# Kernel optimization log

Hardware: AMD Instinct MI355X
Metric: run time of the kernel (lower is better)

The kernel has to match this reference:

```python
import jax, jax.numpy as jnp
import numpy as np


def setup_inputs() -> dict:
    key = jax.random.key(0)
    k1, k2, k3, k4 = jax.random.split(key, 4)
    N, E, DIN, H1, H2 = 100000, 1600000, 128, 64, 32
    x = jax.random.normal(k1, (N, DIN), dtype=jnp.float32)
    edge_index = jax.random.randint(k2, (2, E), 0, N, dtype=jnp.int64)
    # Glorot-style scaled init for the two GCN weight matrices (no bias)
    W1 = jax.random.normal(k3, (DIN, H1), dtype=jnp.float32) * (1.0 / np.sqrt(DIN))
    W2 = jax.random.normal(k4, (H1, H2), dtype=jnp.float32) * (1.0 / np.sqrt(H1))
    return {"x": x, "edge_index": edge_index, "W1": W1, "W2": W2}


def reference(x, edge_index, W1, W2):
    N = x.shape[0]
    loop = jnp.arange(N, dtype=edge_index.dtype)
    src = jnp.concatenate([edge_index[0], loop])  # [E+N]
    dst = jnp.concatenate([edge_index[1], loop])  # [E+N]
    # symmetric GCN normalization with self-loops (edge_weight = 1)
    deg = jax.ops.segment_sum(jnp.ones(src.shape, x.dtype), dst, num_segments=N)
    dinv = jnp.where(deg > 0, jax.lax.rsqrt(deg), 0.0)
    norm = dinv[src] * dinv[dst]  # [E+N]

    def gcn_conv(h, W):
        h = h @ W  # transform first (PyG GCNConv order)
        msg = h[src] * norm[:, None]  # gather + scale
        return jax.ops.segment_sum(msg, dst, num_segments=N)  # scatter-add

    hidden1 = jax.nn.relu(gcn_conv(x, W1))
    z = gcn_conv(hidden1, W2)
    return z
```

## Files before the change

kernel.cpp:

```cpp
#include <hip/hip_runtime.h>
#include <hip/hip_fp16.h>

#define DIN 128
#define H1  64
#define H2  32
#define NCH 512
#define BSH 8

typedef _Float16 f16x8 __attribute__((ext_vector_type(8)));
typedef _Float16 f16x4 __attribute__((ext_vector_type(4)));
typedef float    f32x4 __attribute__((ext_vector_type(4)));

__global__ __launch_bounds__(256) void k_hist(const int* __restrict__ dst,
        int* __restrict__ H, int E, int NB, int chunk) {
    __shared__ int lh[512];
    int c = blockIdx.x, tid = threadIdx.x;
    for (int b = tid; b < NB; b += 256) lh[b] = 0;
    __syncthreads();
    int e0 = c * chunk, e1 = min(E, e0 + chunk);
    for (int e = e0 + tid; e < e1; e += 256)
        atomicAdd(&lh[dst[e] >> BSH], 1);
    __syncthreads();
    for (int b = tid; b < NB; b += 256) H[(size_t)b * NCH + c] = lh[b];
}

__global__ __launch_bounds__(256) void k_scan1(const int* __restrict__ in,
        int* __restrict__ out, int* __restrict__ partial, int N) {
    int tid = threadIdx.x;
    int base = blockIdx.x * 1024 + tid * 4;
    int v0 = (base + 0 < N) ? in[base + 0] : 0;
    int v1 = (base + 1 < N) ? in[base + 1] : 0;
    int v2 = (base + 2 < N) ? in[base + 2] : 0;
    int v3 = (base + 3 < N) ? in[base + 3] : 0;
    int sum = v0 + v1 + v2 + v3;
    int lane = tid & 63, wid = tid >> 6;
    int x = sum;
#pragma unroll
    for (int off = 1; off < 64; off <<= 1) {
        int y = __shfl_up(x, off, 64);
        if (lane >= off) x += y;
    }
    __shared__ int wsum[4];
    if (lane == 63) wsum[wid] = x;
    __syncthreads();
    int wbase = 0;
    for (int w = 0; w < wid; ++w) wbase += wsum[w];
    int excl = wbase + x - sum;
    if (base + 0 < N) out[base + 0] = excl;
    if (base + 1 < N) out[base + 1] = excl + v0;
    if (base + 2 < N) out[base + 2] = excl + v0 + v1;
    if (base + 3 < N) out[base + 3] = excl + v0 + v1 + v2;
    if (tid == 0) partial[blockIdx.x] = wsum[0] + wsum[1] + wsum[2] + wsum[3];
}

__global__ __launch_bounds__(256) void k_scan2(int* __restrict__ partial, int nb) {
    int tid = threadIdx.x;
    int v = (tid < nb) ? partial[tid] : 0;
    __shared__ int tmp[256];
    tmp[tid] = v;
    __syncthreads();
    for (int off = 1; off < 256; off <<= 1) {
        int y = (tid >= off) ? tmp[tid - off] : 0;
        __syncthreads();
        tmp[tid] += y;
        __syncthreads();
    }
    if (tid < nb) partial[tid] = tmp[tid] - v;
}

__global__ void k_scan3b(int* __restrict__ a, const int* __restrict__ partial, int n) {
    int i = blockIdx.x * blockDim.x + threadIdx.x;
    if (i < n) a[i] += partial[i >> 10];
}

__global__ __launch_bounds__(256) void k_bsort(const int* __restrict__ src,
        const int* __restrict__ dst, const int* __restrict__ H,
        int* __restrict__ ep, int E, int NB, int chunk) {
    __shared__ int cur[512];
    int c = blockIdx.x, tid = threadIdx.x;
    for (int b = tid; b < NB; b += 256) cur[b] = H[(size_t)b * NCH + c];
    __syncthreads();
    int e0 = c * chunk, e1 = min(E, e0 + chunk);
    for (int e = e0 + tid; e < e1; e += 256) {
        int s = src[e], d = dst[e];
        int pos = atomicAdd(&cur[d >> BSH], 1);
        ep[pos] = s | ((d & ((1 << BSH) - 1)) << 20);
    }
}

__global__ __launch_bounds__(256) void k_csr(const int* __restrict__ ep,
        const int* __restrict__ H, int* __restrict__ degi, int* __restrict__ rowptr,
        float* __restrict__ dinv, int* __restrict__ csr_src, int E, int N, int NB) {
    __shared__ int cnt[256], pos[256], wsum[4];
    int b = blockIdx.x, tid = threadIdx.x;
    int base = b << BSH;
    cnt[tid] = 0;
    int bstart = H[(size_t)b * NCH];
    int bend = (b + 1 < NB) ? H[(size_t)(b + 1) * NCH] : E;
    __syncthreads();
    for (int e = bstart + tid; e < bend; e += 256)
        atomicAdd(&cnt[ep[e] >> 20], 1);
    __syncthreads();
    int v = cnt[tid];
    int lane = tid & 63, wid = tid >> 6;
    int x = v;
#pragma unroll
    for (int off = 1; off < 64; off <<= 1) {
        int y = __shfl_up(x, off, 64);
        if (lane >= off) x += y;
    }
    if (lane == 63) wsum[wid] = x;
    __syncthreads();
    int wbase = 0;
    for (int w = 0; w < wid; ++w) wbase += wsum[w];
    int excl = wbase + x - v;
    int n = base + tid;
    if (n < N) {
        degi[n]   = v;
        dinv[n]   = rsqrtf((float)v + 1.0f);
        rowptr[n] = bstart + excl;
    }
    pos[tid] = bstart + excl;
    __syncthreads();
    for (int e = bstart + tid; e < bend; e += 256) {
        int p = ep[e];
        int q = atomicAdd(&pos[p >> 20], 1);
        csr_src[q] = p & 0xFFFFF;
    }
}

__global__ __launch_bounds__(256) void k_mgemm1(const float* __restrict__ x,
        const float* __restrict__ W1, const float* __restrict__ dinv,
        _Float16* __restrict__ t1h, int N) {
    __shared__ _Float16 sA[64 * 128];
    __shared__ _Float16 sB[64 * 128];
    int tid = threadIdx.x;
    int row0 = blockIdx.x * 64;
#pragma unroll
    for (int i = 0; i < 8; ++i) {
        int idx4 = tid + 256 * i;
        int r = idx4 >> 5, c4 = idx4 & 31;
        int row = row0 + r;
        float4 v = make_float4(0.f, 0.f, 0.f, 0.f);
        if (row < N) v = *(const float4*)&x[(size_t)row * DIN + c4 * 4];
        f16x4 h;
        h[0] = (_Float16)v.x; h[1] = (_Float16)v.y;
        h[2] = (_Float16)v.z; h[3] = (_Float16)v.w;
        int byte = (c4 * 8) ^ ((r & 7) << 4);
        *(f16x4*)((char*)sA + r * 256 + byte) = h;
    }
    {
        int n = tid & 63, kq = tid >> 6;
        _Float16 tmp[32];
#pragma unroll
        for (int kk = 0; kk < 32; ++kk)
            tmp[kk] = (_Float16)W1[(size_t)(kq * 32 + kk) * H1 + n];
#pragma unroll
        for (int j = 0; j < 4; ++j) {
            int byte = ((kq * 32 + j * 8) * 2) ^ ((n & 7) << 4);
            *(f16x8*)((char*)sB + n * 256 + byte) = *(f16x8*)&tmp[j * 8];
        }
    }
    __syncthreads();
    int lane = tid & 63, w = tid >> 6;
    int lr = lane & 15, kg = lane >> 4;
    f32x4 acc[4] = {};
    int ar = w * 16 + lr;
    const char* pa = (const char*)sA + ar * 256;
    int axor = (ar & 7) << 4;
#pragma unroll
    for (int ks = 0; ks < 4; ++ks) {
        int kb = ks * 64 + kg * 16;
        f16x8 a = *(const f16x8*)(pa + (kb ^ axor));
#pragma unroll
        for (int nt = 0; nt < 4; ++nt) {
            int bn = nt * 16 + lr;
            f16x8 b = *(const f16x8*)((const char*)sB + bn * 256 + (kb ^ ((bn & 7) << 4)));
            acc[nt] = __builtin_amdgcn_mfma_f32_16x16x32_f16(a, b, acc[nt], 0, 0, 0);
        }
    }
#pragma unroll
    for (int rg = 0; rg < 4; ++rg) {
        int R = row0 + w * 16 + kg * 4 + rg;
        if (R < N) {
            float dv = dinv[R];
#pragma unroll
            for (int nt = 0; nt < 4; ++nt)
                t1h[(size_t)R * H1 + nt * 16 + lr] = (_Float16)(acc[nt][rg] * dv);
        }
    }
}

__global__ __launch_bounds__(256) void k_mgemm2(const _Float16* __restrict__ aggh,
        const float* __restrict__ W2, const float* __restrict__ dinv,
        _Float16* __restrict__ t2h, int N) {
    __shared__ _Float16 sA[64 * 64];
    __shared__ _Float16 sB[32 * 64];
    int tid = threadIdx.x;
    int row0 = blockIdx.x * 64;
#pragma unroll
    for (int i = 0; i < 2; ++i) {
        int idx8 = tid + 256 * i;
        int r = idx8 >> 3, c8 = idx8 & 7;
        int row = row0 + r;
        f16x8 h = {};
        if (row < N) h = *(const f16x8*)&aggh[(size_t)row * H1 + c8 * 8];
        int byte = (c8 * 16) ^ ((r & 7) << 4);
        *(f16x8*)((char*)sA + r * 128 + byte) = h;
    }
    {
        int n = tid & 31, kq = tid >> 5;
        _Float16 tmp[8];
#pragma unroll
        for (int kk = 0; kk < 8; ++kk)
            tmp[kk] = (_Float16)W2[(size_t)(kq * 8 + kk) * H2 + n];
        int byte = (kq * 16) ^ ((n & 7) << 4);
        *(f16x8*)((char*)sB + n * 128 + byte) = *(f16x8*)&tmp[0];
    }
    __syncthreads();
    int lane = tid & 63, w = tid >> 6;
    int lr = lane & 15, kg = lane >> 4;
    f32x4 acc[2] = {};
    int ar = w * 16 + lr;
    const char* pa = (const char*)sA + ar * 128;
    int axor = (ar & 7) << 4;
#pragma unroll
    for (int ks = 0; ks < 2; ++ks) {
        int kb = ks * 64 + kg * 16;
        f16x8 a = *(const f16x8*)(pa + (kb ^ axor));
#pragma unroll
        for (int nt = 0; nt < 2; ++nt) {
            int bn = nt * 16 + lr;
            f16x8 b = *(const f16x8*)((const char*)sB + bn * 128 + (kb ^ ((bn & 7) << 4)));
            acc[nt] = __builtin_amdgcn_mfma_f32_16x16x32_f16(a, b, acc[nt], 0, 0, 0);
        }
    }
#pragma unroll
    for (int rg = 0; rg < 4; ++rg) {
        int R = row0 + w * 16 + kg * 4 + rg;
        if (R < N) {
            float dv = dinv[R];
#pragma unroll
            for (int nt = 0; nt < 2; ++nt)
                t2h[(size_t)R * H2 + nt * 16 + lr] = (_Float16)(acc[nt][rg] * dv);
        }
    }
}

template <int LOGF2, bool FUSE>
__global__ __launch_bounds__(256) void k_aggv(const int* __restrict__ rowptr,
        const int* __restrict__ degi, const int* __restrict__ csr_src,
        const float* __restrict__ dinv, const __half2* __restrict__ tp,
        void* __restrict__ outv, int N) {
    const int F2 = 1 << LOGF2;
    int local = threadIdx.x >> LOGF2;
    int j = threadIdx.x & (F2 - 1);
    int n = blockIdx.x * (256 >> LOGF2) + local;
    if (n >= N) return;
    int start = rowptr[n];
    int deg = degi[n];
    float2 f = __half22float2(tp[((size_t)n << LOGF2) + j]);
    float ax = f.x, ay = f.y;
    for (int k = 0; k < deg; k += 8) {
        int raw[8];
#pragma unroll
        for (int u = 0; u < 8; ++u)
            raw[u] = csr_src[start + k + u];
#pragma unroll
        for (int u = 0; u < 8; ++u) {
            bool valid = (k + u) < deg;
            int s = valid ? raw[u] : 0;
            float2 g = __half22float2(tp[((size_t)s << LOGF2) + j]);
            ax += valid ? g.x : 0.f;
            ay += valid ? g.y : 0.f;
        }
    }
    float dv = dinv[n];
    size_t idx = ((size_t)n << LOGF2) + j;
    if (FUSE) {
        ((__half2*)outv)[idx] =
            __floats2half2_rn(fmaxf(ax * dv, 0.f), fmaxf(ay * dv, 0.f));
    } else {
        ((float2*)outv)[idx] = make_float2(ax * dv, ay * dv);
    }
}

extern "C" void kernel_launch(void* const* d_in, const int* in_sizes, int n_in,
                              void* d_out, int out_size, void* d_ws, size_t ws_size,
                              hipStream_t stream) {
    const float* x  = (const float*)d_in[0];
    const int*   ei = (const int*)d_in[1];
    const float* W1 = (const float*)d_in[2];
    const float* W2 = (const float*)d_in[3];

    const int N = in_sizes[0] / DIN;
    const int E = in_sizes[1] / 2;
    const int* src = ei;
    const int* dst = ei + E;

    const int NB    = (N + (1 << BSH) - 1) >> BSH;
    const int NBNCH = NB * NCH;
    const int chunk = (E + NCH - 1) / NCH;

    float*    dinv    = (float*)d_ws;
    int*      degi    = (int*)(dinv + N);
    int*      rowptr  = degi + N;
    int*      H       = rowptr + N;
    int*      partial = H + NBNCH;
    int*      csr_src = partial + 256;
    _Float16* t1h     = (_Float16*)(csr_src + E + 8);
    _Float16* agg1h   = t1h + (size_t)N * H1;
    _Float16* t2h     = t1h;
    float*    out     = (float*)d_out;
    int*      ep      = (int*)t1h;

    k_hist<<<NCH, 256, 0, stream>>>(dst, H, E, NB, chunk);
    k_scan1<<<(NBNCH + 1023) / 1024, 256, 0, stream>>>(H, H, partial, NBNCH);
    k_scan2<<<1, 256, 0, stream>>>(partial, (NBNCH + 1023) / 1024);
    k_scan3b<<<(NBNCH + 255) / 256, 256, 0, stream>>>(H, partial, NBNCH);
    k_bsort<<<NCH, 256, 0, stream>>>(src, dst, H, ep, E, NB, chunk);
    k_csr<<<NB, 256, 0, stream>>>(ep, H, degi, rowptr, dinv, csr_src, E, N, NB);

    const int ntile = (N + 63) / 64;

    k_mgemm1<<<ntile, 256, 0, stream>>>(x, W1, dinv, t1h, N);
    k_aggv<5, true><<<(N + 7) / 8, 256, 0, stream>>>(rowptr, degi, csr_src, dinv,
                                                     (const __half2*)t1h, agg1h, N);

    k_mgemm2<<<ntile, 256, 0, stream>>>(agg1h, W2, dinv, t2h, N);
    k_aggv<4, false><<<(N + 15) / 16, 256, 0, stream>>>(rowptr, degi, csr_src, dinv,
                                                        (const __half2*)t2h, out, N);
}
```

Measured before the change: 145.5 us.

## Split feature matrices into 16-column panels and aggregate per panel

The GEMM outputs t1h/t2h and agg1h are now stored panel-major: separate N×16 half panels instead of row-major N×64/N×32. Aggregation runs as a 2D grid with one panel per blockIdx.y, so each gathered row is a 32-byte chunk and each panel's working set (about 3.2 MB) is smaller and more cache-friendly. The trade-off is that the CSR index list is re-read once per panel and each gather brings in less data per random access.

```diff
diff --git a/kernel.cpp b/kernel.cpp
--- a/kernel.cpp
+++ b/kernel.cpp
@@ -186,7 +186,8 @@
             float dv = dinv[R];
 #pragma unroll
             for (int nt = 0; nt < 4; ++nt)
-                t1h[(size_t)R * H1 + nt * 16 + lr] = (_Float16)(acc[nt][rg] * dv);
+                t1h[(size_t)nt * N * 16 + (size_t)R * 16 + lr] =
+                    (_Float16)(acc[nt][rg] * dv);
         }
     }
 }
@@ -204,7 +205,10 @@
         int r = idx8 >> 3, c8 = idx8 & 7;
         int row = row0 + r;
         f16x8 h = {};
-        if (row < N) h = *(const f16x8*)&aggh[(size_t)row * H1 + c8 * 8];
+        if (row < N) {
+            int q = c8 >> 1, h8 = c8 & 1;
+            h = *(const f16x8*)&aggh[(size_t)q * N * 16 + (size_t)row * 16 + h8 * 8];
+        }
         int byte = (c8 * 16) ^ ((r & 7) << 4);
         *(f16x8*)((char*)sA + r * 128 + byte) = h;
     }
@@ -242,24 +246,26 @@
             float dv = dinv[R];
 #pragma unroll
             for (int nt = 0; nt < 2; ++nt)
-                t2h[(size_t)R * H2 + nt * 16 + lr] = (_Float16)(acc[nt][rg] * dv);
-        }
-    }
-}
-
-template <int LOGF2, bool FUSE>
-__global__ __launch_bounds__(256) void k_aggv(const int* __restrict__ rowptr,
+                t2h[(size_t)nt * N * 16 + (size_t)R * 16 + lr] =
+                    (_Float16)(acc[nt][rg] * dv);
+        }
+    }
+}
+
+template <bool FUSE>
+__global__ __launch_bounds__(256) void k_aggp(const int* __restrict__ rowptr,
         const int* __restrict__ degi, const int* __restrict__ csr_src,
-        const float* __restrict__ dinv, const __half2* __restrict__ tp,
+        const float* __restrict__ dinv, const __half2* __restrict__ tph,
         void* __restrict__ outv, int N) {
-    const int F2 = 1 << LOGF2;
-    int local = threadIdx.x >> LOGF2;
-    int j = threadIdx.x & (F2 - 1);
-    int n = blockIdx.x * (256 >> LOGF2) + local;
+    int q = blockIdx.y;
+    const __half2* tp = tph + (size_t)q * N * 8;
+    int local = threadIdx.x >> 3;
+    int j = threadIdx.x & 7;
+    int n = blockIdx.x * 32 + local;
     if (n >= N) return;
     int start = rowptr[n];
     int deg = degi[n];
-    float2 f = __half22float2(tp[((size_t)n << LOGF2) + j]);
+    float2 f = __half22float2(tp[(size_t)n * 8 + j]);
     float ax = f.x, ay = f.y;
     for (int k = 0; k < deg; k += 8) {
         int raw[8];
@@ -270,18 +276,18 @@
         for (int u = 0; u < 8; ++u) {
             bool valid = (k + u) < deg;
             int s = valid ? raw[u] : 0;
-            float2 g = __half22float2(tp[((size_t)s << LOGF2) + j]);
+            float2 g = __half22float2(tp[(size_t)s * 8 + j]);
             ax += valid ? g.x : 0.f;
             ay += valid ? g.y : 0.f;
         }
     }
     float dv = dinv[n];
-    size_t idx = ((size_t)n << LOGF2) + j;
     if (FUSE) {
-        ((__half2*)outv)[idx] =
+        ((__half2*)outv)[(size_t)q * N * 8 + (size_t)n * 8 + j] =
             __floats2half2_rn(fmaxf(ax * dv, 0.f), fmaxf(ay * dv, 0.f));
     } else {
-        ((float2*)outv)[idx] = make_float2(ax * dv, ay * dv);
+        ((float2*)outv)[(size_t)n * 16 + (size_t)q * 8 + j] =
+            make_float2(ax * dv, ay * dv);
     }
 }
 
@@ -322,12 +328,19 @@
     k_csr<<<NB, 256, 0, stream>>>(ep, H, degi, rowptr, dinv, csr_src, E, N, NB);
 
     const int ntile = (N + 63) / 64;
+    const int nagg  = (N + 31) / 32;
 
     k_mgemm1<<<ntile, 256, 0, stream>>>(x, W1, dinv, t1h, N);
-    k_aggv<5, true><<<(N + 7) / 8, 256, 0, stream>>>(rowptr, degi, csr_src, dinv,
-                                                     (const __half2*)t1h, agg1h, N);
+    {
+        dim3 g(nagg, 4);
+        k_aggp<true><<<g, 256, 0, stream>>>(rowptr, degi, csr_src, dinv,
+                                            (const __half2*)t1h, agg1h, N);
+    }
 
     k_mgemm2<<<ntile, 256, 0, stream>>>(agg1h, W2, dinv, t2h, N);
-    k_aggv<4, false><<<(N + 15) / 16, 256, 0, stream>>>(rowptr, degi, csr_src, dinv,
-                                                        (const __half2*)t2h, out, N);
-}
+    {
+        dim3 g(nagg, 2);
+        k_aggp<false><<<g, 256, 0, stream>>>(rowptr, degi, csr_src, dinv,
+                                             (const __half2*)t2h, out, N);
+    }
+}
```

Measured after the change: 138.7 us. -4.7%, faster.

## Pad CSR rows to multiples of 8 and gather 16-byte feature vectors

Applied to the files above, without the earlier changes.

Splits CSR construction into count, block-scan and fill kernels so that every row's neighbour list is padded to a multiple of 8. Padding entries point to an extra zeroed sentinel row N in the feature buffers, which the GEMM kernels clear. The aggregation kernel now reads indices with int4 loads, drops the per-edge validity predication, and has each lane gather 8 halfs (16 bytes) at a time, so fewer lanes serve each node. This is meant to raise memory-level parallelism and cut instruction count in the gather. In exchange it adds two launches, pad writes and extra workspace, and the padding adds wasted gathers, worst for low-degree nodes.

```diff
diff --git a/kernel.cpp b/kernel.cpp
--- a/kernel.cpp
+++ b/kernel.cpp
@@ -88,12 +88,11 @@
     }
 }
 
-__global__ __launch_bounds__(256) void k_csr(const int* __restrict__ ep,
-        const int* __restrict__ H, int* __restrict__ degi, int* __restrict__ rowptr,
-        float* __restrict__ dinv, int* __restrict__ csr_src, int E, int N, int NB) {
-    __shared__ int cnt[256], pos[256], wsum[4];
+__global__ __launch_bounds__(256) void k_csrA(const int* __restrict__ ep,
+        const int* __restrict__ H, int* __restrict__ degi, float* __restrict__ dinv,
+        int* __restrict__ lexcl, int* __restrict__ btot, int E, int N, int NB) {
+    __shared__ int cnt[256], wsum[4];
     int b = blockIdx.x, tid = threadIdx.x;
-    int base = b << BSH;
     cnt[tid] = 0;
     int bstart = H[(size_t)b * NCH];
     int bend = (b + 1 < NB) ? H[(size_t)(b + 1) * NCH] : E;
@@ -102,8 +101,10 @@
         atomicAdd(&cnt[ep[e] >> 20], 1);
     __syncthreads();
     int v = cnt[tid];
+    int n = (b << BSH) + tid;
+    int d8 = (n < N) ? ((v + 7) & ~7) : 0;
     int lane = tid & 63, wid = tid >> 6;
-    int x = v;
+    int x = d8;
 #pragma unroll
     for (int off = 1; off < 64; off <<= 1) {
         int y = __shfl_up(x, off, 64);
@@ -113,19 +114,61 @@
     __syncthreads();
     int wbase = 0;
     for (int w = 0; w < wid; ++w) wbase += wsum[w];
-    int excl = wbase + x - v;
-    int n = base + tid;
+    int excl = wbase + x - d8;
     if (n < N) {
-        degi[n]   = v;
-        dinv[n]   = rsqrtf((float)v + 1.0f);
-        rowptr[n] = bstart + excl;
-    }
-    pos[tid] = bstart + excl;
+        degi[n]  = v;
+        dinv[n]  = rsqrtf((float)v + 1.0f);
+        lexcl[n] = excl;
+    }
+    if (tid == 0) btot[b] = wsum[0] + wsum[1] + wsum[2] + wsum[3];
+}
+
+__global__ __launch_bounds__(256) void k_scanC(int* __restrict__ a, int nb) {
+    int tid = threadIdx.x;
+    int i0 = 2 * tid, i1 = 2 * tid + 1;
+    int v0 = (i0 < nb) ? a[i0] : 0;
+    int v1 = (i1 < nb) ? a[i1] : 0;
+    int p = v0 + v1;
+    __shared__ int tmp[256];
+    tmp[tid] = p;
+    __syncthreads();
+    for (int off = 1; off < 256; off <<= 1) {
+        int y = (tid >= off) ? tmp[tid - off] : 0;
+        __syncthreads();
+        tmp[tid] += y;
+        __syncthreads();
+    }
+    int excl = tmp[tid] - p;
+    if (i0 < nb) a[i0] = excl;
+    if (i1 < nb) a[i1] = excl + v0;
+}
+
+__global__ __launch_bounds__(256) void k_csrB(const int* __restrict__ ep,
+        const int* __restrict__ H, const int* __restrict__ degi,
+        const int* __restrict__ bbase, const int* __restrict__ lexcl,
+        int* __restrict__ rowptr, int* __restrict__ csr_src, int E, int N, int NB) {
+    __shared__ int pos[256];
+    int b = blockIdx.x, tid = threadIdx.x;
+    int bstart = H[(size_t)b * NCH];
+    int bend = (b + 1 < NB) ? H[(size_t)(b + 1) * NCH] : E;
+    int n = (b << BSH) + tid;
+    int startv = 0;
+    if (n < N) {
+        startv = bbase[b] + lexcl[n];
+        rowptr[n] = startv;
+    }
+    pos[tid] = startv;
     __syncthreads();
     for (int e = bstart + tid; e < bend; e += 256) {
         int p = ep[e];
         int q = atomicAdd(&pos[p >> 20], 1);
         csr_src[q] = p & 0xFFFFF;
+    }
+    __syncthreads();
+    if (n < N) {
+        int d = degi[n], d8 = (d + 7) & ~7;
+        for (int z = startv + d; z < startv + d8; ++z)
+            csr_src[z] = N;
     }
 }
 
@@ -136,6 +179,8 @@
     __shared__ _Float16 sB[64 * 128];
     int tid = threadIdx.x;
     int row0 = blockIdx.x * 64;
+    if (blockIdx.x == 0 && tid < 8)
+        ((f32x4*)(t1h + (size_t)N * H1))[tid] = (f32x4){0.f, 0.f, 0.f, 0.f};
 #pragma unroll
     for (int i = 0; i < 8; ++i) {
         int idx4 = tid + 256 * i;
@@ -198,6 +243,8 @@
     __shared__ _Float16 sB[32 * 64];
     int tid = threadIdx.x;
     int row0 = blockIdx.x * 64;
+    if (blockIdx.x == 0 && tid < 4)
+        ((f32x4*)(t2h + (size_t)N * H2))[tid] = (f32x4){0.f, 0.f, 0.f, 0.f};
 #pragma unroll
     for (int i = 0; i < 2; ++i) {
         int idx8 = tid + 256 * i;
@@ -247,41 +294,49 @@
     }
 }
 
-template <int LOGF2, bool FUSE>
-__global__ __launch_bounds__(256) void k_aggv(const int* __restrict__ rowptr,
+template <int LOGL, bool FUSE>
+__global__ __launch_bounds__(256) void k_aggq(const int* __restrict__ rowptr,
         const int* __restrict__ degi, const int* __restrict__ csr_src,
-        const float* __restrict__ dinv, const __half2* __restrict__ tp,
+        const float* __restrict__ dinv, const _Float16* __restrict__ tp,
         void* __restrict__ outv, int N) {
-    const int F2 = 1 << LOGF2;
-    int local = threadIdx.x >> LOGF2;
-    int j = threadIdx.x & (F2 - 1);
-    int n = blockIdx.x * (256 >> LOGF2) + local;
+    const int L = 1 << LOGL;
+    const int F = L * 8;
+    int local = threadIdx.x >> LOGL;
+    int j = threadIdx.x & (L - 1);
+    int n = blockIdx.x * (256 >> LOGL) + local;
     if (n >= N) return;
     int start = rowptr[n];
     int deg = degi[n];
-    float2 f = __half22float2(tp[((size_t)n << LOGF2) + j]);
-    float ax = f.x, ay = f.y;
+    f16x8 sv = *(const f16x8*)&tp[(size_t)n * F + j * 8];
+    float acc[8];
+#pragma unroll
+    for (int t = 0; t < 8; ++t) acc[t] = (float)sv[t];
     for (int k = 0; k < deg; k += 8) {
-        int raw[8];
+        int4 ra = *(const int4*)&csr_src[start + k];
+        int4 rb = *(const int4*)&csr_src[start + k + 4];
+        int idx[8] = {ra.x, ra.y, ra.z, ra.w, rb.x, rb.y, rb.z, rb.w};
+        f16x8 g[8];
 #pragma unroll
         for (int u = 0; u < 8; ++u)
-            raw[u] = csr_src[start + k + u];
-#pragma unroll
-        for (int u = 0; u < 8; ++u) {
-            bool valid = (k + u) < deg;
-            int s = valid ? raw[u] : 0;
-            float2 g = __half22float2(tp[((size_t)s << LOGF2) + j]);
-            ax += valid ? g.x : 0.f;
-            ay += valid ? g.y : 0.f;
-        }
+            g[u] = *(const f16x8*)&tp[(size_t)idx[u] * F + j * 8];
+#pragma unroll
+        for (int u = 0; u < 8; ++u)
+#pragma unroll
+            for (int t = 0; t < 8; ++t)
+                acc[t] += (float)g[u][t];
     }
     float dv = dinv[n];
-    size_t idx = ((size_t)n << LOGF2) + j;
     if (FUSE) {
-        ((__half2*)outv)[idx] =
-            __floats2half2_rn(fmaxf(ax * dv, 0.f), fmaxf(ay * dv, 0.f));
+        f16x8 o;
+#pragma unroll
+        for (int t = 0; t < 8; ++t) o[t] = (_Float16)fmaxf(acc[t] * dv, 0.f);
+        *(f16x8*)((_Float16*)outv + (size_t)n * F + j * 8) = o;
     } else {
-        ((float2*)outv)[idx] = make_float2(ax * dv, ay * dv);
+        float* op = (float*)outv + (size_t)n * F + j * 8;
+        f32x4 o0 = {acc[0] * dv, acc[1] * dv, acc[2] * dv, acc[3] * dv};
+        f32x4 o1 = {acc[4] * dv, acc[5] * dv, acc[6] * dv, acc[7] * dv};
+        *(f32x4*)op = o0;
+        *(f32x4*)(op + 4) = o1;
     }
 }
 
@@ -305,11 +360,13 @@
     float*    dinv    = (float*)d_ws;
     int*      degi    = (int*)(dinv + N);
     int*      rowptr  = degi + N;
-    int*      H       = rowptr + N;
+    int*      lexcl   = rowptr + N;
+    int*      H       = lexcl + N;
     int*      partial = H + NBNCH;
-    int*      csr_src = partial + 256;
-    _Float16* t1h     = (_Float16*)(csr_src + E + 8);
-    _Float16* agg1h   = t1h + (size_t)N * H1;
+    int*      btot    = partial + 256;
+    int*      csr_src = btot + 512;
+    _Float16* t1h     = (_Float16*)(csr_src + E + 8 * N);
+    _Float16* agg1h   = t1h + (size_t)(N + 1) * H1;
     _Float16* t2h     = t1h;
     float*    out     = (float*)d_out;
     int*      ep      = (int*)t1h;
@@ -319,15 +376,17 @@
     k_scan2<<<1, 256, 0, stream>>>(partial, (NBNCH + 1023) / 1024);
     k_scan3b<<<(NBNCH + 255) / 256, 256, 0, stream>>>(H, partial, NBNCH);
     k_bsort<<<NCH, 256, 0, stream>>>(src, dst, H, ep, E, NB, chunk);
-    k_csr<<<NB, 256, 0, stream>>>(ep, H, degi, rowptr, dinv, csr_src, E, N, NB);
+    k_csrA<<<NB, 256, 0, stream>>>(ep, H, degi, dinv, lexcl, btot, E, N, NB);
+    k_scanC<<<1, 256, 0, stream>>>(btot, NB);
+    k_csrB<<<NB, 256, 0, stream>>>(ep, H, degi, btot, lexcl, rowptr, csr_src, E, N, NB);
 
     const int ntile = (N + 63) / 64;
 
     k_mgemm1<<<ntile, 256, 0, stream>>>(x, W1, dinv, t1h, N);
-    k_aggv<5, true><<<(N + 7) / 8, 256, 0, stream>>>(rowptr, degi, csr_src, dinv,
-                                                     (const __half2*)t1h, agg1h, N);
+    k_aggq<3, true><<<(N + 31) / 32, 256, 0, stream>>>(rowptr, degi, csr_src, dinv,
+                                                       t1h, agg1h, N);
 
     k_mgemm2<<<ntile, 256, 0, stream>>>(agg1h, W2, dinv, t2h, N);
-    k_aggv<4, false><<<(N + 15) / 16, 256, 0, stream>>>(rowptr, degi, csr_src, dinv,
-                                                        (const __half2*)t2h, out, N);
-}
+    k_aggq<2, false><<<(N + 63) / 64, 256, 0, stream>>>(rowptr, degi, csr_src, dinv,
+                                                        t2h, out, N);
+}
```

Measured after the change: 128.5 us (median of 2 runs). -11.7%, faster.
